# Kernel tuning notes

Hardware: AMD Instinct MI355X
Metric: run time of the kernel (lower is better)

The kernel has to match this reference:

```python
import jax, jax.numpy as jnp
import numpy as np

NUM_AGENTS = 64
IN_FEATURES = 512
OUT_FEATURES = 512
BATCH = 2048


def setup_inputs() -> dict:
    key = jax.random.key(0)
    k1, k2, k3, k4 = jax.random.split(key, 4)
    which_agents = jax.random.randint(k1, (BATCH,), 0, NUM_AGENTS, dtype=jnp.int64 if jax.config.jax_enable_x64 else jnp.int32)
    x = jax.random.normal(k2, (BATCH, IN_FEATURES), dtype=jnp.float32)
    # kaiming_uniform_(a=sqrt(5)) -> bound = sqrt(6 / ((1 + 5) * fan_in)) = 1/sqrt(fan_in)
    bound_w = 1.0 / np.sqrt(IN_FEATURES)
    weight = jax.random.uniform(k3, (NUM_AGENTS, OUT_FEATURES, IN_FEATURES), jnp.float32, -bound_w, bound_w)
    bound_b = 1.0 / np.sqrt(IN_FEATURES)
    bias = jax.random.uniform(k4, (NUM_AGENTS, OUT_FEATURES), jnp.float32, -bound_b, bound_b)
    return {"which_agents": which_agents, "input": x, "weight": weight, "bias": bias}


def reference(which_agents, input, weight, bias):
    # weight[which_agents]: [B, out, in]; batched matvec with input [B, in]
    w = weight[which_agents]          # [B, O, I]
    b = bias[which_agents]            # [B, O]
    return jnp.einsum('boi,bi->bo', w, input) + b
```

## Files before the change

### kernel.cpp

```cpp
#include <hip/hip_runtime.h>


constexpr int BATCH  = 2048;
constexpr int NAGENT = 64;
constexpr int IN_F   = 512;
constexpr int OUT_F  = 512;

constexpr int BN  = 128;
constexpr int MCH = 64;
constexpr int XS  = IN_F + 8;

typedef __attribute__((ext_vector_type(8))) short short8;
typedef __attribute__((ext_vector_type(4))) float f32x4;

__device__ inline unsigned short f2bf(float f) {
  unsigned u = __float_as_uint(f);
  return (unsigned short)((u + 0x7FFFu + ((u >> 16) & 1u)) >> 16);
}

__global__ __launch_bounds__(512, 2) void agent_linear_mfma(
    const int*   __restrict__ which,
    const float* __restrict__ x,
    const float* __restrict__ weight,
    const float* __restrict__ bias,
    float*       __restrict__ out) {
  const int tid   = threadIdx.x;
  const int lane  = tid & 63;
  const int wid   = tid >> 6;
  const int agent = blockIdx.y;
  const int obase = blockIdx.x * BN;

  __shared__ int rowlist_s[BATCH];
  __shared__ int wsum_s[8];
  __shared__ __align__(16) unsigned short Xs[MCH * XS];

  int4 v = ((const int4*)which)[tid];
  int lc = (v.x == agent) + (v.y == agent) + (v.z == agent) + (v.w == agent);
  int s = lc;
#pragma unroll
  for (int off = 1; off < 64; off <<= 1) {
    int t = __shfl_up(s, off);
    if (lane >= off) s += t;
  }
  if (lane == 63) wsum_s[wid] = s;
  __syncthreads();
  int base = 0, count = 0;
#pragma unroll
  for (int w = 0; w < 8; ++w) {
    int ws = wsum_s[w];
    if (w < wid) base += ws;
    count += ws;
  }
  {
    int pos = base + s - lc;
    if (v.x == agent) rowlist_s[pos++] = 4 * tid + 0;
    if (v.y == agent) rowlist_s[pos++] = 4 * tid + 1;
    if (v.z == agent) rowlist_s[pos++] = 4 * tid + 2;
    if (v.w == agent) rowlist_s[pos++] = 4 * tid + 3;
  }
  __syncthreads();

  const int nl = lane & 15;
  const int kq = lane >> 4;

  const float* wp = weight + ((size_t)agent * OUT_F + obase + wid * 16 + nl) * IN_F + kq * 8;
  const float  bv = bias[agent * OUT_F + obase + wid * 16 + nl];

  for (int m0 = 0; m0 < count; m0 += MCH) {
    const int mcount = min(MCH, count - m0);

    __syncthreads();
#pragma unroll 4
    for (int it = 0; it < MCH / 4; ++it) {
      int r = it * 4 + (tid >> 7);
      int c = (tid & 127) * 4;
      float4 xv = {0.f, 0.f, 0.f, 0.f};
      if (r < mcount) xv = *(const float4*)(x + (size_t)rowlist_s[m0 + r] * IN_F + c);
      unsigned lo = (unsigned)f2bf(xv.x) | ((unsigned)f2bf(xv.y) << 16);
      unsigned hi = (unsigned)f2bf(xv.z) | ((unsigned)f2bf(xv.w) << 16);
      uint2 w2 = {lo, hi};
      *(uint2*)&Xs[r * XS + c] = w2;
    }
    __syncthreads();

    f32x4 acc[4] = {{0.f, 0.f, 0.f, 0.f}, {0.f, 0.f, 0.f, 0.f},
                    {0.f, 0.f, 0.f, 0.f}, {0.f, 0.f, 0.f, 0.f}};
    float4 b0 = *(const float4*)(wp);
    float4 b1 = *(const float4*)(wp + 4);
    for (int kc = 0; kc < IN_F; kc += 32) {
      float4 c0 = b0, c1 = b1;
      int kn = kc + 32;
      if (kn < IN_F) {
        b0 = *(const float4*)(wp + kn);
        b1 = *(const float4*)(wp + kn + 4);
      }
      short8 bf;
      bf[0] = (short)f2bf(c0.x); bf[1] = (short)f2bf(c0.y);
      bf[2] = (short)f2bf(c0.z); bf[3] = (short)f2bf(c0.w);
      bf[4] = (short)f2bf(c1.x); bf[5] = (short)f2bf(c1.y);
      bf[6] = (short)f2bf(c1.z); bf[7] = (short)f2bf(c1.w);
#pragma unroll
      for (int i = 0; i < 4; ++i) {
        short8 af = *(const short8*)&Xs[(i * 16 + nl) * XS + kc + kq * 8];
        acc[i] = __builtin_amdgcn_mfma_f32_16x16x32_bf16(af, bf, acc[i], 0, 0, 0);
      }
    }

#pragma unroll
    for (int i = 0; i < 4; ++i) {
#pragma unroll
      for (int r = 0; r < 4; ++r) {
        int ml = i * 16 + kq * 4 + r;
        if (ml < mcount) {
          int grow = rowlist_s[m0 + ml];
          out[(size_t)grow * OUT_F + obase + wid * 16 + nl] = acc[i][r] + bv;
        }
      }
    }
  }
}

extern "C" void kernel_launch(void* const* d_in, const int* in_sizes, int n_in,
                              void* d_out, int out_size, void* d_ws, size_t ws_size,
                              hipStream_t stream) {
  const int*   which = (const int*)d_in[0];
  const float* x     = (const float*)d_in[1];
  const float* w     = (const float*)d_in[2];
  const float* b     = (const float*)d_in[3];
  float*       out   = (float*)d_out;

  dim3 grid(OUT_F / BN, NAGENT);
  agent_linear_mfma<<<grid, dim3(512), 0, stream>>>(which, x, w, b, out);
}
```

Before: 109.9 us.

## Split K across two wave groups with 1024-thread blocks and LDS reduction

Doubles the block to 1024 threads and splits the 512-wide reduction dimension between two groups of 8 waves. Each group handles half of K, and the partial sums are combined through a shared-memory buffer before the output write. The intent is more waves in flight to hide weight-load latency, plus a fully unrolled, double-buffered weight prefetch with packed bf16 conversion. The cost is an extra LDS reduction and barrier per M chunk, plus more shared memory, which may limit occupancy. The weight tile is still re-read for every M chunk.

```diff
diff --git a/kernel.cpp b/kernel.cpp
--- a/kernel.cpp
+++ b/kernel.cpp
@@ -12,13 +12,17 @@
 
 typedef __attribute__((ext_vector_type(8))) short short8;
 typedef __attribute__((ext_vector_type(4))) float f32x4;
+typedef __attribute__((ext_vector_type(4))) unsigned int u32x4;
 
-__device__ inline unsigned short f2bf(float f) {
+__device__ inline unsigned rnd_bf(float f) {
   unsigned u = __float_as_uint(f);
-  return (unsigned short)((u + 0x7FFFu + ((u >> 16) & 1u)) >> 16);
+  return u + 0x7FFFu + ((u >> 16) & 1u);
+}
+__device__ inline unsigned pk_bf(float lo, float hi) {
+  return (rnd_bf(lo) >> 16) | (rnd_bf(hi) & 0xFFFF0000u);
 }
 
-__global__ __launch_bounds__(512, 2) void agent_linear_mfma(
+__global__ __launch_bounds__(1024, 4) void agent_linear_mfma2(
     const int*   __restrict__ which,
     const float* __restrict__ x,
     const float* __restrict__ weight,
@@ -27,15 +31,18 @@
   const int tid   = threadIdx.x;
   const int lane  = tid & 63;
   const int wid   = tid >> 6;
+  const int w8    = wid & 7;
+  const int kh    = wid >> 3;
   const int agent = blockIdx.y;
   const int obase = blockIdx.x * BN;
 
   __shared__ int rowlist_s[BATCH];
-  __shared__ int wsum_s[8];
+  __shared__ int wsum_s[16];
   __shared__ __align__(16) unsigned short Xs[MCH * XS];
+  __shared__ float Rs[8][MCH][17];
 
-  int4 v = ((const int4*)which)[tid];
-  int lc = (v.x == agent) + (v.y == agent) + (v.z == agent) + (v.w == agent);
+  int2 v = ((const int2*)which)[tid];
+  int lc = (v.x == agent) + (v.y == agent);
   int s = lc;
 #pragma unroll
   for (int off = 1; off < 64; off <<= 1) {
@@ -46,74 +53,86 @@
   __syncthreads();
   int base = 0, count = 0;
 #pragma unroll
-  for (int w = 0; w < 8; ++w) {
+  for (int w = 0; w < 16; ++w) {
     int ws = wsum_s[w];
     if (w < wid) base += ws;
     count += ws;
   }
   {
     int pos = base + s - lc;
-    if (v.x == agent) rowlist_s[pos++] = 4 * tid + 0;
-    if (v.y == agent) rowlist_s[pos++] = 4 * tid + 1;
-    if (v.z == agent) rowlist_s[pos++] = 4 * tid + 2;
-    if (v.w == agent) rowlist_s[pos++] = 4 * tid + 3;
+    if (v.x == agent) rowlist_s[pos++] = 2 * tid;
+    if (v.y == agent) rowlist_s[pos]   = 2 * tid + 1;
   }
-  __syncthreads();
 
   const int nl = lane & 15;
   const int kq = lane >> 4;
 
-  const float* wp = weight + ((size_t)agent * OUT_F + obase + wid * 16 + nl) * IN_F + kq * 8;
-  const float  bv = bias[agent * OUT_F + obase + wid * 16 + nl];
+  const float* wp = weight + ((size_t)(agent * OUT_F + obase + w8 * 16 + nl)) * IN_F
+                  + kh * 256 + kq * 8;
+  const float  bv = bias[agent * OUT_F + obase + w8 * 16 + nl];
 
   for (int m0 = 0; m0 < count; m0 += MCH) {
     const int mcount = min(MCH, count - m0);
+    __syncthreads();
 
-    __syncthreads();
-#pragma unroll 4
-    for (int it = 0; it < MCH / 4; ++it) {
-      int r = it * 4 + (tid >> 7);
-      int c = (tid & 127) * 4;
-      float4 xv = {0.f, 0.f, 0.f, 0.f};
-      if (r < mcount) xv = *(const float4*)(x + (size_t)rowlist_s[m0 + r] * IN_F + c);
-      unsigned lo = (unsigned)f2bf(xv.x) | ((unsigned)f2bf(xv.y) << 16);
-      unsigned hi = (unsigned)f2bf(xv.z) | ((unsigned)f2bf(xv.w) << 16);
-      uint2 w2 = {lo, hi};
-      *(uint2*)&Xs[r * XS + c] = w2;
+#pragma unroll
+    for (int t = 0; t < 8; ++t) {
+      int idx = t * 1024 + tid;
+      int r   = idx >> 7;
+      int c4  = idx & 127;
+      uint2 w2 = {0u, 0u};
+      if (r < mcount) {
+        float4 xv = *(const float4*)(x + (size_t)rowlist_s[m0 + r] * IN_F + c4 * 4);
+        w2.x = pk_bf(xv.x, xv.y);
+        w2.y = pk_bf(xv.z, xv.w);
+      }
+      *(uint2*)&Xs[r * XS + c4 * 4] = w2;
     }
     __syncthreads();
 
-    f32x4 acc[4] = {{0.f, 0.f, 0.f, 0.f}, {0.f, 0.f, 0.f, 0.f},
-                    {0.f, 0.f, 0.f, 0.f}, {0.f, 0.f, 0.f, 0.f}};
-    float4 b0 = *(const float4*)(wp);
-    float4 b1 = *(const float4*)(wp + 4);
-    for (int kc = 0; kc < IN_F; kc += 32) {
-      float4 c0 = b0, c1 = b1;
-      int kn = kc + 32;
-      if (kn < IN_F) {
-        b0 = *(const float4*)(wp + kn);
-        b1 = *(const float4*)(wp + kn + 4);
+    f32x4 acc[4] = {{0.f,0.f,0.f,0.f},{0.f,0.f,0.f,0.f},
+                    {0.f,0.f,0.f,0.f},{0.f,0.f,0.f,0.f}};
+    const int kbase = kh * 256;
+    float4 pa[2], pb[2];
+    pa[0] = *(const float4*)(wp);      pb[0] = *(const float4*)(wp + 4);
+    pa[1] = *(const float4*)(wp + 32); pb[1] = *(const float4*)(wp + 36);
+#pragma unroll
+    for (int k = 0; k < 8; ++k) {
+      float4 c0 = pa[k & 1], c1 = pb[k & 1];
+      if (k + 2 < 8) {
+        pa[k & 1] = *(const float4*)(wp + (k + 2) * 32);
+        pb[k & 1] = *(const float4*)(wp + (k + 2) * 32 + 4);
       }
-      short8 bf;
-      bf[0] = (short)f2bf(c0.x); bf[1] = (short)f2bf(c0.y);
-      bf[2] = (short)f2bf(c0.z); bf[3] = (short)f2bf(c0.w);
-      bf[4] = (short)f2bf(c1.x); bf[5] = (short)f2bf(c1.y);
-      bf[6] = (short)f2bf(c1.z); bf[7] = (short)f2bf(c1.w);
+      u32x4 q;
+      q[0] = pk_bf(c0.x, c0.y); q[1] = pk_bf(c0.z, c0.w);
+      q[2] = pk_bf(c1.x, c1.y); q[3] = pk_bf(c1.z, c1.w);
+      short8 bf = __builtin_bit_cast(short8, q);
 #pragma unroll
       for (int i = 0; i < 4; ++i) {
-        short8 af = *(const short8*)&Xs[(i * 16 + nl) * XS + kc + kq * 8];
+        short8 af = *(const short8*)&Xs[(i * 16 + nl) * XS + kbase + k * 32 + kq * 8];
         acc[i] = __builtin_amdgcn_mfma_f32_16x16x32_bf16(af, bf, acc[i], 0, 0, 0);
       }
     }
 
+    if (kh == 1) {
 #pragma unroll
-    for (int i = 0; i < 4; ++i) {
+      for (int i = 0; i < 4; ++i)
 #pragma unroll
-      for (int r = 0; r < 4; ++r) {
-        int ml = i * 16 + kq * 4 + r;
-        if (ml < mcount) {
-          int grow = rowlist_s[m0 + ml];
-          out[(size_t)grow * OUT_F + obase + wid * 16 + nl] = acc[i][r] + bv;
+        for (int r = 0; r < 4; ++r)
+          Rs[w8][i * 16 + kq * 4 + r][nl] = acc[i][r];
+    }
+    __syncthreads();
+
+    if (kh == 0) {
+#pragma unroll
+      for (int i = 0; i < 4; ++i) {
+#pragma unroll
+        for (int r = 0; r < 4; ++r) {
+          int m = i * 16 + kq * 4 + r;
+          if (m < mcount) {
+            out[(size_t)rowlist_s[m0 + m] * OUT_F + obase + w8 * 16 + nl] =
+                acc[i][r] + Rs[w8][m][nl] + bv;
+          }
         }
       }
     }
@@ -130,5 +149,5 @@
   float*       out   = (float*)d_out;
 
   dim3 grid(OUT_F / BN, NAGENT);
-  agent_linear_mfma<<<grid, dim3(512), 0, stream>>>(which, x, w, b, out);
+  agent_linear_mfma2<<<grid, dim3(1024), 0, stream>>>(which, x, w, b, out);
 }
```

Result: no change. 107.9 us (-1.8%).
